# Kernel optimization log

Measured on AMD Instinct MI355X. Metric: run time of the kernel, lower is better.

The kernel has to match this reference:

```python
import jax, jax.numpy as jnp
import numpy as np

N, INSIZE, K, D = 512, 512, 64, 16


def setup_inputs() -> dict:
    key = jax.random.key(0)
    k1, k2, k3 = jax.random.split(key, 3)
    x = jax.random.normal(k1, (N, INSIZE), dtype=jnp.float32)
    W = jax.random.normal(k2, (K * D, INSIZE), dtype=jnp.float32) * (1.0 / np.sqrt(INSIZE))
    b = jax.random.normal(k3, (K * D,), dtype=jnp.float32) * 0.01
    return {"x": x, "W": W, "b": b}


def reference(x, W, b):
    # Linear: [N, insize] -> [N, K*D] -> [N, K, D]
    feat = (x @ W.T + b).reshape(-1, K, D)
    n = feat.shape[0]
    # Pairwise L1 distance over D: norm[i, k, j] = sum_d |feat[i,k,d] - feat[j,k,d]|
    # feature [N,K,D,1] vs feature_ [1,K,D,N] in the original broadcast
    diff = jnp.abs(feat[:, :, :, None] - jnp.transpose(feat, (1, 2, 0))[None])  # [N,K,D,N]
    norm = jnp.sum(diff, axis=2)  # [N,K,N]
    # Eraser: suppress self-similarity on the diagonal with a large penalty
    eraser = jnp.eye(n, dtype=feat.dtype)[:, None, :]  # [N,1,N]
    c_b = jnp.exp(-(norm + eraser * 1e6))
    o_b = jnp.sum(c_b, axis=2)  # [N,K]
    return jnp.concatenate((x, o_b), axis=1)  # [N, insize+K]
```

## Files before the change

### kernel.cpp

```cpp
#include <hip/hip_runtime.h>

#define NPTS 512
#define INS  512
#define KDIM 64
#define DDIM 16
#define CDIM (KDIM*DDIM)
#define OUTC (INS + KDIM)
#define KSPLIT 4
#define FEAT_ELEMS ((size_t)NPTS * CDIM)
#define LOG2E 1.4426950408889634f

typedef short short8 __attribute__((ext_vector_type(8)));
typedef float f32x4  __attribute__((ext_vector_type(4)));

__device__ __forceinline__ float exp2_fast(float x) {
    return __builtin_amdgcn_exp2f(x);
}

__device__ __forceinline__ unsigned int f2bf(float f) {
    unsigned int x = __float_as_uint(f);
    return (x + 0x7fffu + ((x >> 16) & 1u)) >> 16;
}

__device__ __forceinline__ uint4 cvt8(const float* src) {
    float4 lo = *(const float4*)src;
    float4 hi = *(const float4*)(src + 4);
    uint4 v;
    v.x = f2bf(lo.x) | (f2bf(lo.y) << 16);
    v.y = f2bf(lo.z) | (f2bf(lo.w) << 16);
    v.z = f2bf(hi.x) | (f2bf(hi.y) << 16);
    v.w = f2bf(hi.z) | (f2bf(hi.w) << 16);
    return v;
}

__global__ __launch_bounds__(256) void prepack_kernel(
    const float* __restrict__ x, const float* __restrict__ W,
    uint4* __restrict__ xP, uint4* __restrict__ WP, float* __restrict__ out)
{
    const int b = blockIdx.x;
    if (b < 128) {
        const int t = b * 256 + threadIdx.x;
        const int kc = t & 63, i = t >> 6;
        xP[kc * NPTS + i] = cvt8(x + i * INS + kc * 8);
    } else if (b < 384) {
        const int t = (b - 128) * 256 + threadIdx.x;
        const int kc = t & 63, c = t >> 6;
        WP[kc * CDIM + c] = cvt8(W + c * INS + kc * 8);
    } else {
        const int idx = (b - 384) * 256 + threadIdx.x;
        const int i  = idx / (OUTC / 4);
        const int j4 = idx - i * (OUTC / 4);
        float4 v;
        if (j4 < INS / 4) v = ((const float4*)x)[i * (INS / 4) + j4];
        else              v = make_float4(-1.0f, -1.0f, -1.0f, -1.0f);
        ((float4*)out)[idx] = v;
    }
}

__global__ __launch_bounds__(256) void mfma_gemm_kernel(
    const uint4* __restrict__ xP, const uint4* __restrict__ WP,
    const float* __restrict__ bias, float* __restrict__ featT)
{
    __shared__ uint4 As[16 * 64];
    __shared__ uint4 Bs[16 * 64];

    const int tid   = threadIdx.x;
    const int cbase = blockIdx.x * 64;
    const int ibase = blockIdx.y * 64;
    const int kc0   = blockIdx.z * 16;

    #pragma unroll
    for (int r = 0; r < 4; ++r) {
        const int idx = r * 256 + tid;
        const int kc = idx >> 6, col = idx & 63;
        As[idx] = xP[(kc0 + kc) * NPTS + ibase + col];
        Bs[idx] = WP[(kc0 + kc) * CDIM + cbase + col];
    }
    __syncthreads();

    const int lane = tid & 63, wv = tid >> 6;
    const int quad = lane >> 4, ln = lane & 15;

    f32x4 acc[4];
    #pragma unroll
    for (int mi = 0; mi < 4; ++mi) acc[mi] = (f32x4){0.f, 0.f, 0.f, 0.f};

    #pragma unroll
    for (int t = 0; t < 4; ++t) {
        uint4 bu = Bs[(t * 4 + quad) * 64 + wv * 16 + ln];
        short8 bf = *(short8*)&bu;
        #pragma unroll
        for (int mi = 0; mi < 4; ++mi) {
            uint4 au = As[(t * 4 + quad) * 64 + mi * 16 + ln];
            short8 af = *(short8*)&au;
            acc[mi] = __builtin_amdgcn_mfma_f32_16x16x32_bf16(af, bf, acc[mi], 0, 0, 0);
        }
    }

    const int kg = (cbase >> 4) + wv;
    float badd = 0.f;
    if (blockIdx.z == 0) badd = bias[cbase + wv * 16 + ln];
    float* dst = featT + (size_t)blockIdx.z * FEAT_ELEMS
               + ((size_t)kg * NPTS) * DDIM + ln;
    #pragma unroll
    for (int mi = 0; mi < 4; ++mi) {
        #pragma unroll
        for (int reg = 0; reg < 4; ++reg) {
            const int i = ibase + mi * 16 + quad * 4 + reg;
            dst[(size_t)i * DDIM] = (acc[mi][reg] + badd) * LOG2E;
        }
    }
}

__device__ __forceinline__ float4 sum4(const float4* s0, const float4* s1,
                                       const float4* s2, const float4* s3, size_t g) {
    float4 a = s0[g], b = s1[g], c = s2[g], d = s3[g];
    float4 r;
    r.x = (a.x + b.x) + (c.x + d.x);
    r.y = (a.y + b.y) + (c.y + d.y);
    r.z = (a.z + b.z) + (c.z + d.z);
    r.w = (a.w + b.w) + (c.w + d.w);
    return r;
}

__global__ __launch_bounds__(256, 4) void pairwise_kernel(
    const float* __restrict__ f0, const float* __restrict__ f1,
    const float* __restrict__ f2, const float* __restrict__ f3,
    float* __restrict__ out)
{
    const int k     = blockIdx.x;
    const int itile = blockIdx.y;
    const int jq    = blockIdx.z;

    __shared__ float4 fj4[64 * 4];
    __shared__ float4 fiL[16 * 64];
    __shared__ float  part[4][256];

    const float4* s0 = (const float4*)f0;
    const float4* s1 = (const float4*)f1;
    const float4* s2 = (const float4*)f2;
    const float4* s3 = (const float4*)f3;

    {
        const size_t g = ((size_t)k * NPTS + jq * 64) * 4 + threadIdx.x;
        fj4[threadIdx.x] = sum4(s0, s1, s2, s3, g);
    }
    {
        const size_t base = ((size_t)k * NPTS + itile * 256) * 4;
        #pragma unroll
        for (int r = 0; r < 4; ++r) {
            const int idx = r * 256 + threadIdx.x;
            const int il = idx >> 2, q = idx & 3;
            fiL[((il >> 6) * 4 + q) * 64 + (il & 63)] = sum4(s0, s1, s2, s3, base + idx);
        }
    }
    __syncthreads();

    const int lane = threadIdx.x & 63;
    const int wv   = threadIdx.x >> 6;

    float fi[4][16];
    #pragma unroll
    for (int u = 0; u < 4; ++u) {
        #pragma unroll
        for (int q = 0; q < 4; ++q) {
            float4 v = fiL[(u * 4 + q) * 64 + lane];
            fi[u][q * 4 + 0] = v.x; fi[u][q * 4 + 1] = v.y;
            fi[u][q * 4 + 2] = v.z; fi[u][q * 4 + 3] = v.w;
        }
    }

    float acc[4] = {0.f, 0.f, 0.f, 0.f};
    const float4* fp = fj4 + wv * 16 * 4;
    #pragma unroll 2
    for (int jj = 0; jj < 16; ++jj) {
        float4 q0 = fp[jj * 4 + 0];
        float4 q1 = fp[jj * 4 + 1];
        float4 q2 = fp[jj * 4 + 2];
        float4 q3 = fp[jj * 4 + 3];
        #pragma unroll
        for (int u = 0; u < 4; ++u) {
            float a0 = fabsf(fi[u][0]  - q0.x) + fabsf(fi[u][1]  - q0.y)
                     + fabsf(fi[u][2]  - q0.z) + fabsf(fi[u][3]  - q0.w);
            float a1 = fabsf(fi[u][4]  - q1.x) + fabsf(fi[u][5]  - q1.y)
                     + fabsf(fi[u][6]  - q1.z) + fabsf(fi[u][7]  - q1.w);
            float a2 = fabsf(fi[u][8]  - q2.x) + fabsf(fi[u][9]  - q2.y)
                     + fabsf(fi[u][10] - q2.z) + fabsf(fi[u][11] - q2.w);
            float a3 = fabsf(fi[u][12] - q3.x) + fabsf(fi[u][13] - q3.y)
                     + fabsf(fi[u][14] - q3.z) + fabsf(fi[u][15] - q3.w);
            acc[u] += exp2_fast(-((a0 + a1) + (a2 + a3)));
        }
    }

    #pragma unroll
    for (int u = 0; u < 4; ++u)
        part[wv][u * 64 + lane] = acc[u];
    __syncthreads();

    {
        const int t = threadIdx.x;
        float s = (part[0][t] + part[1][t]) + (part[2][t] + part[3][t]);
        const int i = itile * 256 + t;
        atomicAdd(&out[(size_t)i * OUTC + INS + k], s);
    }
}

extern "C" void kernel_launch(void* const* d_in, const int* in_sizes, int n_in,
                              void* d_out, int out_size, void* d_ws, size_t ws_size,
                              hipStream_t stream) {
    const float* x    = (const float*)d_in[0];
    const float* W    = (const float*)d_in[1];
    const float* bias = (const float*)d_in[2];
    float* out = (float*)d_out;

    float* featT = (float*)d_ws;
    uint4* xP = (uint4*)(featT + KSPLIT * FEAT_ELEMS);
    uint4* WP = xP + 64 * NPTS;

    prepack_kernel<<<dim3(672), 256, 0, stream>>>(x, W, xP, WP, out);
    mfma_gemm_kernel<<<dim3(16, 8, 4), 256, 0, stream>>>(xP, WP, bias, featT);
    pairwise_kernel<<<dim3(KDIM, 2, 8), 256, 0, stream>>>(
        featT, featT + FEAT_ELEMS, featT + 2 * FEAT_ELEMS, featT + 3 * FEAT_ELEMS, out);
}
```

Before: 101.0 us.

## Drop split-K GEMM partials and load features directly in pairwise kernel

The GEMM no longer splits K four ways into separate partial buffers. Each block now covers the full reduction on smaller 32x32 output tiles, launched as 512 blocks. The pairwise kernel no longer reads and sums four partial feature buffers; it reads one feature buffer, loading the i-side rows straight into registers and skipping the shared staging. This removes about three quarters of the feature write and read traffic, at the cost of a longer serial MFMA chain per wave and less reuse of each shared tile in the GEMM.

```diff
diff --git a/kernel.cpp b/kernel.cpp
--- a/kernel.cpp
+++ b/kernel.cpp
@@ -6,8 +6,6 @@
 #define DDIM 16
 #define CDIM (KDIM*DDIM)
 #define OUTC (INS + KDIM)
-#define KSPLIT 4
-#define FEAT_ELEMS ((size_t)NPTS * CDIM)
 #define LOG2E 1.4426950408889634f
 
 typedef short short8 __attribute__((ext_vector_type(8)));
@@ -59,73 +57,49 @@
 
 __global__ __launch_bounds__(256) void mfma_gemm_kernel(
     const uint4* __restrict__ xP, const uint4* __restrict__ WP,
-    const float* __restrict__ bias, float* __restrict__ featT)
+    const float* __restrict__ bias, float* __restrict__ featR)
 {
-    __shared__ uint4 As[16 * 64];
-    __shared__ uint4 Bs[16 * 64];
+    __shared__ uint4 As[64 * 32];
+    __shared__ uint4 Bs[64 * 32];
 
     const int tid   = threadIdx.x;
-    const int cbase = blockIdx.x * 64;
-    const int ibase = blockIdx.y * 64;
-    const int kc0   = blockIdx.z * 16;
+    const int cbase = blockIdx.x * 32;
+    const int ibase = blockIdx.y * 32;
 
     #pragma unroll
-    for (int r = 0; r < 4; ++r) {
+    for (int r = 0; r < 8; ++r) {
         const int idx = r * 256 + tid;
-        const int kc = idx >> 6, col = idx & 63;
-        As[idx] = xP[(kc0 + kc) * NPTS + ibase + col];
-        Bs[idx] = WP[(kc0 + kc) * CDIM + cbase + col];
+        const int kc = idx >> 5, col = idx & 31;
+        As[idx] = xP[kc * NPTS + ibase + col];
+        Bs[idx] = WP[kc * CDIM + cbase + col];
     }
     __syncthreads();
 
     const int lane = tid & 63, wv = tid >> 6;
     const int quad = lane >> 4, ln = lane & 15;
+    const int mi = wv & 1, ci = wv >> 1;
 
-    f32x4 acc[4];
+    f32x4 acc = (f32x4){0.f, 0.f, 0.f, 0.f};
     #pragma unroll
-    for (int mi = 0; mi < 4; ++mi) acc[mi] = (f32x4){0.f, 0.f, 0.f, 0.f};
-
-    #pragma unroll
-    for (int t = 0; t < 4; ++t) {
-        uint4 bu = Bs[(t * 4 + quad) * 64 + wv * 16 + ln];
-        short8 bf = *(short8*)&bu;
-        #pragma unroll
-        for (int mi = 0; mi < 4; ++mi) {
-            uint4 au = As[(t * 4 + quad) * 64 + mi * 16 + ln];
-            short8 af = *(short8*)&au;
-            acc[mi] = __builtin_amdgcn_mfma_f32_16x16x32_bf16(af, bf, acc[mi], 0, 0, 0);
-        }
+    for (int t = 0; t < 16; ++t) {
+        short8 af = *(short8*)&As[(t * 4 + quad) * 32 + mi * 16 + ln];
+        short8 bf = *(short8*)&Bs[(t * 4 + quad) * 32 + ci * 16 + ln];
+        acc = __builtin_amdgcn_mfma_f32_16x16x32_bf16(af, bf, acc, 0, 0, 0);
     }
 
-    const int kg = (cbase >> 4) + wv;
-    float badd = 0.f;
-    if (blockIdx.z == 0) badd = bias[cbase + wv * 16 + ln];
-    float* dst = featT + (size_t)blockIdx.z * FEAT_ELEMS
-               + ((size_t)kg * NPTS) * DDIM + ln;
+    const int c  = cbase + ci * 16 + ln;
+    const int kg = c >> 4;
+    const float badd = bias[c];
+    float* dst = featR + ((size_t)kg * NPTS) * DDIM + ln;
     #pragma unroll
-    for (int mi = 0; mi < 4; ++mi) {
-        #pragma unroll
-        for (int reg = 0; reg < 4; ++reg) {
-            const int i = ibase + mi * 16 + quad * 4 + reg;
-            dst[(size_t)i * DDIM] = (acc[mi][reg] + badd) * LOG2E;
-        }
+    for (int reg = 0; reg < 4; ++reg) {
+        const int i = ibase + mi * 16 + quad * 4 + reg;
+        dst[(size_t)i * DDIM] = (acc[reg] + badd) * LOG2E;
     }
 }
 
-__device__ __forceinline__ float4 sum4(const float4* s0, const float4* s1,
-                                       const float4* s2, const float4* s3, size_t g) {
-    float4 a = s0[g], b = s1[g], c = s2[g], d = s3[g];
-    float4 r;
-    r.x = (a.x + b.x) + (c.x + d.x);
-    r.y = (a.y + b.y) + (c.y + d.y);
-    r.z = (a.z + b.z) + (c.z + d.z);
-    r.w = (a.w + b.w) + (c.w + d.w);
-    return r;
-}
-
 __global__ __launch_bounds__(256, 4) void pairwise_kernel(
-    const float* __restrict__ f0, const float* __restrict__ f1,
-    const float* __restrict__ f2, const float* __restrict__ f3,
+    const float* __restrict__ featR,
     float* __restrict__ out)
 {
     const int k     = blockIdx.x;
@@ -133,28 +107,10 @@
     const int jq    = blockIdx.z;
 
     __shared__ float4 fj4[64 * 4];
-    __shared__ float4 fiL[16 * 64];
     __shared__ float  part[4][256];
 
-    const float4* s0 = (const float4*)f0;
-    const float4* s1 = (const float4*)f1;
-    const float4* s2 = (const float4*)f2;
-    const float4* s3 = (const float4*)f3;
-
-    {
-        const size_t g = ((size_t)k * NPTS + jq * 64) * 4 + threadIdx.x;
-        fj4[threadIdx.x] = sum4(s0, s1, s2, s3, g);
-    }
-    {
-        const size_t base = ((size_t)k * NPTS + itile * 256) * 4;
-        #pragma unroll
-        for (int r = 0; r < 4; ++r) {
-            const int idx = r * 256 + threadIdx.x;
-            const int il = idx >> 2, q = idx & 3;
-            fiL[((il >> 6) * 4 + q) * 64 + (il & 63)] = sum4(s0, s1, s2, s3, base + idx);
-        }
-    }
-    __syncthreads();
+    fj4[threadIdx.x] =
+        ((const float4*)featR)[((size_t)k * NPTS + jq * 64) * 4 + threadIdx.x];
 
     const int lane = threadIdx.x & 63;
     const int wv   = threadIdx.x >> 6;
@@ -162,13 +118,15 @@
     float fi[4][16];
     #pragma unroll
     for (int u = 0; u < 4; ++u) {
-        #pragma unroll
-        for (int q = 0; q < 4; ++q) {
-            float4 v = fiL[(u * 4 + q) * 64 + lane];
-            fi[u][q * 4 + 0] = v.x; fi[u][q * 4 + 1] = v.y;
-            fi[u][q * 4 + 2] = v.z; fi[u][q * 4 + 3] = v.w;
-        }
+        const int i = itile * 256 + u * 64 + lane;
+        const float4* p = (const float4*)(featR + ((size_t)k * NPTS + i) * DDIM);
+        float4 v0 = p[0], v1 = p[1], v2 = p[2], v3 = p[3];
+        fi[u][0]=v0.x;  fi[u][1]=v0.y;  fi[u][2]=v0.z;  fi[u][3]=v0.w;
+        fi[u][4]=v1.x;  fi[u][5]=v1.y;  fi[u][6]=v1.z;  fi[u][7]=v1.w;
+        fi[u][8]=v2.x;  fi[u][9]=v2.y;  fi[u][10]=v2.z; fi[u][11]=v2.w;
+        fi[u][12]=v3.x; fi[u][13]=v3.y; fi[u][14]=v3.z; fi[u][15]=v3.w;
     }
+    __syncthreads();
 
     float acc[4] = {0.f, 0.f, 0.f, 0.f};
     const float4* fp = fj4 + wv * 16 * 4;
@@ -213,12 +171,11 @@
     const float* bias = (const float*)d_in[2];
     float* out = (float*)d_out;
 
-    float* featT = (float*)d_ws;
-    uint4* xP = (uint4*)(featT + KSPLIT * FEAT_ELEMS);
+    float* featR = (float*)d_ws;
+    uint4* xP = (uint4*)(featR + (size_t)NPTS * CDIM);
     uint4* WP = xP + 64 * NPTS;
 
     prepack_kernel<<<dim3(672), 256, 0, stream>>>(x, W, xP, WP, out);
-    mfma_gemm_kernel<<<dim3(16, 8, 4), 256, 0, stream>>>(xP, WP, bias, featT);
-    pairwise_kernel<<<dim3(KDIM, 2, 8), 256, 0, stream>>>(
-        featT, featT + FEAT_ELEMS, featT + 2 * FEAT_ELEMS, featT + 3 * FEAT_ELEMS, out);
+    mfma_gemm_kernel<<<dim3(CDIM / 32, NPTS / 32), 256, 0, stream>>>(xP, WP, bias, featR);
+    pairwise_kernel<<<dim3(KDIM, 2, 8), 256, 0, stream>>>(featR, out);
 }
```

Measured after the change: 98.59 us. -2.3%, faster.
